# Kernel tuning notes

Measured on AMD Instinct MI355X. Metric: run time of the kernel, lower is better.

## Reference

```python
import jax, jax.numpy as jnp
import numpy as np

EPS = 1e-06


def setup_inputs() -> dict:
    key = jax.random.key(0)
    k1, k2, k3 = jax.random.split(key, 3)
    N, L, H, D = 2, 2048, 8, 64
    return {
        "queries": jax.random.normal(k1, (N, L, H, D), dtype=jnp.float32),
        "keys": jax.random.normal(k2, (N, L, H, D), dtype=jnp.float32),
        "values": jax.random.normal(k3, (N, L, H, D), dtype=jnp.float32),
    }


def reference(queries, keys, values):
    # [N, L, H, D] -> [N, H, L, D]
    q = jnp.transpose(queries, (0, 2, 1, 3))
    k = jnp.transpose(keys, (0, 2, 1, 3))
    v = jnp.transpose(values, (0, 2, 1, 3))
    # kernel_method = sigmoid (applied to q and k only)
    q = jax.nn.sigmoid(q)
    k = jax.nn.sigmoid(k)
    L = q.shape[2]
    normal = (jnp.arange(L, dtype=q.dtype) + 1.0)[None, None, :]  # [1,1,L]

    sink_incoming = 1.0 / jnp.einsum('nhld,nhld->nhl', q + EPS, jnp.cumsum(k, axis=2) + EPS)
    source_outgoing = 1.0 / jnp.einsum('nhld,nhld->nhl', k + EPS, jnp.cumsum(q, axis=2) + EPS)
    sink_incoming = sink_incoming * normal
    source_outgoing = source_outgoing * normal

    conserved_sink = jnp.einsum(
        'nhld,nhld->nhl', q + EPS,
        jnp.cumsum(k * source_outgoing[..., None], axis=2) + EPS) / normal
    conserved_source = jnp.einsum(
        'nhld,nhld->nhl', k + EPS,
        jnp.cumsum(q * sink_incoming[..., None], axis=2) + EPS) / normal
    conserved_source = jnp.clip(conserved_source, -1.0, 1.0)

    sink_allocation = jax.nn.sigmoid(conserved_sink)
    conserved_source = jnp.exp(conserved_source)
    source_competition = conserved_source / jnp.cumsum(conserved_source, axis=-1) * normal

    # causal dot product: outer-product cumsum as in the original
    q_scaled = q * (sink_incoming / normal)[..., None]
    v_scaled = v * source_competition[..., None]
    kv = jnp.cumsum(jnp.einsum('nhld,nhlm->nhldm', k, v_scaled), axis=2)  # [N,H,L,D,M]
    qkv = jnp.einsum('nhld,nhldm->nhlm', q_scaled, kv)
    x = qkv * sink_allocation[..., None]
    # back to [N, L, H, M]
    return jnp.transpose(x, (0, 2, 1, 3))
```

## Files before the change

kernel.cpp:

```cpp
#include <hip/hip_runtime.h>
#include <math.h>

constexpr int Nn = 2, Hh = 8, Ll = 2048, Dd = 64;
constexpr int S  = Nn * Hh;
constexpr int C  = 64;
constexpr int NC = Ll / C;
constexpr int SC = S * NC;

constexpr int SB  = 72;
constexpr int SRP = 65;
constexpr int SS8 = 9;

#define EPSF 1e-6f

typedef __attribute__((ext_vector_type(8))) short short8;
typedef __attribute__((ext_vector_type(4))) float f32x4;
#define MFMA16(a, b, c) __builtin_amdgcn_mfma_f32_16x16x32_bf16(a, b, c, 0, 0, 0)

__device__ __forceinline__ float rcpf(float x) { return __builtin_amdgcn_rcpf(x); }
__device__ __forceinline__ float sigf(float x) { return rcpf(1.0f + __expf(-x)); }

__device__ __forceinline__ float waveRed(float v) {
#pragma unroll
    for (int off = 32; off > 0; off >>= 1) v += __shfl_xor(v, off, 64);
    return v;
}

__device__ __forceinline__ int gidx(int n, int l, int h, int d) {
    return ((n * Ll + l) * Hh + h) * Dd + d;
}

__device__ __forceinline__ float fc(const float4& v, int u) { return ((const float*)&v)[u]; }

__device__ __forceinline__ unsigned short f2bf(float x) {
    unsigned int u = __float_as_uint(x);
    unsigned int r = (u + 0x7fffu + ((u >> 16) & 1u)) >> 16;
    return (unsigned short)r;
}
__device__ __forceinline__ unsigned int pack2(float lo, float hi) {
    return (unsigned int)f2bf(lo) | ((unsigned int)f2bf(hi) << 16);
}
__device__ __forceinline__ float bf2f(unsigned short u) {
    return __uint_as_float(((unsigned int)u) << 16);
}
__device__ __forceinline__ float lo16(unsigned int x) { return __uint_as_float(x << 16); }
__device__ __forceinline__ float hi16(unsigned int x) { return __uint_as_float(x & 0xffff0000u); }
__device__ __forceinline__ void unpack8(const uint4& v, float* o) {
    o[0] = lo16(v.x); o[1] = hi16(v.x); o[2] = lo16(v.y); o[3] = hi16(v.y);
    o[4] = lo16(v.z); o[5] = hi16(v.z); o[6] = lo16(v.w); o[7] = hi16(v.w);
}

__global__ __launch_bounds__(256) void k_stage(const float* __restrict__ Q,
                                               const float* __restrict__ K,
                                               const float* __restrict__ V,
                                               unsigned short* __restrict__ Qb,
                                               unsigned short* __restrict__ Kb,
                                               unsigned short* __restrict__ Kt,
                                               unsigned short* __restrict__ Vt,
                                               float* __restrict__ SK,
                                               float* __restrict__ SQ) {
    __shared__ __align__(16) unsigned short skL[C * SB];
    __shared__ float scr[2048];
    int b = blockIdx.x, s = b / NC, c = b % NC;
    int n = s / Hh, h = s % Hh, t = threadIdx.x;
    int d0 = (4 * t) & 63, ig = t >> 4;
    size_t base = (size_t)b * 4096;
    float psk[4] = {0, 0, 0, 0}, psq[4] = {0, 0, 0, 0};
#pragma unroll
    for (int j = 0; j < 4; j++) {
        int i = ig + 16 * j;
        int id = gidx(n, c * C + i, h, d0);
        float4 q4 = *(const float4*)&Q[id];
        float4 k4 = *(const float4*)&K[id];
        float a0 = sigf(q4.x), a1 = sigf(q4.y), a2 = sigf(q4.z), a3 = sigf(q4.w);
        float b0 = sigf(k4.x), b1 = sigf(k4.y), b2 = sigf(k4.z), b3 = sigf(k4.w);
        uint2 pq2 = make_uint2(pack2(a0, a1), pack2(a2, a3));
        uint2 pk2 = make_uint2(pack2(b0, b1), pack2(b2, b3));
        *(uint2*)&Qb[base + i * 64 + d0] = pq2;
        *(uint2*)&Kb[base + i * 64 + d0] = pk2;
        *(uint2*)&skL[i * SB + d0] = pk2;
        psq[0] += a0; psq[1] += a1; psq[2] += a2; psq[3] += a3;
        psk[0] += b0; psk[1] += b1; psk[2] += b2; psk[3] += b3;
    }
#pragma unroll
    for (int r = 0; r < 4; r++) {
        scr[ig * 64 + d0 + r] = psk[r];
        scr[1024 + ig * 64 + d0 + r] = psq[r];
    }
    __syncthreads();
    if (t < 64) {
        float v = 0.f;
        for (int g = 0; g < 16; g++) v += scr[g * 64 + t];
        SK[b * 64 + t] = v;
    } else if (t < 128) {
        int d = t - 64; float v = 0.f;
        for (int g = 0; g < 16; g++) v += scr[1024 + g * 64 + d];
        SQ[b * 64 + d] = v;
    }
    {
        int i0 = (t & 15) * 4, dt = (t >> 4) * 4;
        uint2 kr[4]; float4 vr[4];
#pragma unroll
        for (int r = 0; r < 4; r++) {
            kr[r] = *(const uint2*)&skL[(i0 + r) * SB + dt];
            vr[r] = *(const float4*)&V[gidx(n, c * C + i0 + r, h, dt)];
        }
#pragma unroll
        for (int u = 0; u < 4; u++) {
            unsigned int e0 = (u < 2 ? kr[0].x : kr[0].y), e1 = (u < 2 ? kr[1].x : kr[1].y);
            unsigned int e2 = (u < 2 ? kr[2].x : kr[2].y), e3 = (u < 2 ? kr[3].x : kr[3].y);
            int sh = (u & 1) * 16;
            unsigned int lo = ((e0 >> sh) & 0xffffu) | (((e1 >> sh) & 0xffffu) << 16);
            unsigned int hi = ((e2 >> sh) & 0xffffu) | (((e3 >> sh) & 0xffffu) << 16);
            *(uint2*)&Kt[base + (dt + u) * 64 + i0] = make_uint2(lo, hi);
            *(uint2*)&Vt[base + (dt + u) * 64 + i0] = make_uint2(
                pack2(fc(vr[0], u), fc(vr[1], u)), pack2(fc(vr[2], u), fc(vr[3], u)));
        }
    }
}

__global__ __launch_bounds__(256) void k_pass1(const unsigned short* __restrict__ Qb,
                                               const unsigned short* __restrict__ Kb,
                                               const float* __restrict__ SK,
                                               const float* __restrict__ SQ,
                                               float* __restrict__ SKso,
                                               float* __restrict__ SQsi,
                                               float* __restrict__ si_g,
                                               float* __restrict__ rw1_g,
                                               float* __restrict__ rw2_g) {
    __shared__ __align__(16) unsigned short sqB[C * SB];
    __shared__ __align__(16) unsigned short skB[C * SB];
    __shared__ float P[C * SRP];
    __shared__ float scrA[C * SS8], scrB[C * SS8];
    __shared__ float colK[C], colQ[C], pk[Dd], pq[Dd], lsi[C], lso[C];
    int b = blockIdx.x, s = b / NC, c = b % NC, t = threadIdx.x;
    size_t base = (size_t)b * 4096;

#pragma unroll
    for (int j = 0; j < 2; j++) {
        int flat = 8 * t + 2048 * j, i = flat >> 6, d0 = flat & 63;
        uint4 xq = *(const uint4*)&Qb[base + flat];
        uint4 xk = *(const uint4*)&Kb[base + flat];
        *(uint4*)&sqB[i * SB + d0] = xq;
        *(uint4*)&skB[i * SB + d0] = xk;
        float qa[8], ka[8];
        unpack8(xq, qa); unpack8(xk, ka);
        float sq = 0.f, sk = 0.f;
#pragma unroll
        for (int u = 0; u < 8; u++) { sq += qa[u]; sk += ka[u]; }
        scrB[i * SS8 + (d0 >> 3)] = sq;
        scrA[i * SS8 + (d0 >> 3)] = sk;
    }
    {
        int d = t & 63, g = t >> 6;
        float pa = 0.f, pb = 0.f;
        for (int cp = g; cp < c; cp += 4) {
            pa += SK[(s * NC + cp) * 64 + d];
            pb += SQ[(s * NC + cp) * 64 + d];
        }
        P[2048 + g * 64 + d] = pa;
        P[2304 + g * 64 + d] = pb;
    }
    __syncthreads();
    if (t < 64) {
        float v = 0.f;
#pragma unroll
        for (int u = 0; u < 8; u++) v += scrA[t * SS8 + u];
        colK[t] = v;
    } else if (t < 128) {
        int i = t - 64; float v = 0.f;
#pragma unroll
        for (int u = 0; u < 8; u++) v += scrB[i * SS8 + u];
        colQ[i] = v;
    } else if (t < 192) {
        int d = t - 128;
        pk[d] = P[2048 + d] + P[2112 + d] + P[2176 + d] + P[2240 + d];
    } else {
        int d = t - 192;
        pq[d] = P[2304 + d] + P[2368 + d] + P[2432 + d] + P[2496 + d];
    }
    __syncthreads();

    {
        int w = t >> 6, lane = t & 63, m = lane & 15, q = lane >> 4;
        f32x4 acc[4] = {{0,0,0,0},{0,0,0,0},{0,0,0,0},{0,0,0,0}};
#pragma unroll
        for (int kk = 0; kk < 64; kk += 32) {
            short8 a = *(const short8*)&sqB[(16 * w + m) * SB + kk + q * 8];
#pragma unroll
            for (int J = 0; J < 4; J++) {
                short8 bb = *(const short8*)&skB[(16 * J + m) * SB + kk + q * 8];
                acc[J] = MFMA16(a, bb, acc[J]);
            }
        }
#pragma unroll
        for (int J = 0; J < 4; J++)
#pragma unroll
            for (int r = 0; r < 4; r++)
                P[(16 * w + 4 * q + r) * SRP + 16 * J + m] = acc[J][r];
    }
    __syncthreads();

    {
        int i = t >> 2, g = t & 3, l = c * C + i;
        float r1 = 0.f, r2 = 0.f;
        for (int jj = g; jj <= i; jj += 4) {
            r1 += P[i * SRP + jj] + EPSF * colK[jj];
            r2 += P[jj * SRP + i] + EPSF * colQ[jj];
        }
        float b1 = 0.f, b2 = 0.f;
#pragma unroll
        for (int u = 0; u < 16; u++) {
            int d = g * 16 + u;
            b1 += (bf2f(sqB[i * SB + d]) + EPSF) * (pk[d] + EPSF);
            b2 += (bf2f(skB[i * SB + d]) + EPSF) * (pq[d] + EPSF);
        }
        r1 += __shfl_xor(r1, 1, 64); r1 += __shfl_xor(r1, 2, 64);
        r2 += __shfl_xor(r2, 1, 64); r2 += __shfl_xor(r2, 2, 64);
        b1 += __shfl_xor(b1, 1, 64); b1 += __shfl_xor(b1, 2, 64);
        b2 += __shfl_xor(b2, 1, 64); b2 += __shfl_xor(b2, 2, 64);
        if (g == 0) {
            float nf = (float)(l + 1);
            float siF = nf * rcpf(b1 + r1), soF = nf * rcpf(b2 + r2);
            si_g[s * Ll + l] = siF;
            lsi[i] = siF; lso[i] = soF;
        }
    }
    __syncthreads();

    {
        int i = t >> 2, g = t & 3;
        float a1 = 0.f, a2 = 0.f;
        for (int jj = g; jj <= i; jj += 4) {
            a1 += lso[jj] * (P[i * SRP + jj] + EPSF * colK[jj]);
            a2 += lsi[jj] * (P[jj * SRP + i] + EPSF * colQ[jj]);
        }
        a1 += __shfl_xor(a1, 1, 64); a1 += __shfl_xor(a1, 2, 64);
        a2 += __shfl_xor(a2, 1, 64); a2 += __shfl_xor(a2, 2, 64);
        if (g == 0) {
            rw1_g[s * Ll + c * C + i] = a1;
            rw2_g[s * Ll + c * C + i] = a2;
        }
    }
    {
        int d = t >> 2, g = t & 3;
        float v1 = 0.f, v2 = 0.f;
#pragma unroll
        for (int u = 0; u < 16; u++) {
            int i = g * 16 + u;
            v1 += bf2f(skB[i * SB + d]) * lso[i];
            v2 += bf2f(sqB[i * SB + d]) * lsi[i];
        }
        v1 += __shfl_xor(v1, 1, 64); v1 += __shfl_xor(v1, 2, 64);
        v2 += __shfl_xor(v2, 1, 64); v2 += __shfl_xor(v2, 2, 64);
        if (g == 0) {
            SKso[b * 64 + d] = v1;
            SQsi[b * 64 + d] = v2;
        }
    }
}

__global__ __launch_bounds__(256) void k_pass2(const unsigned short* __restrict__ Qb,
                                               const unsigned short* __restrict__ Kb,
                                               const float* __restrict__ SKso,
                                               const float* __restrict__ SQsi,
                                               const float* __restrict__ si_g,
                                               const float* __restrict__ rw1_g,
                                               const float* __restrict__ rw2_g,
                                               float* __restrict__ s2_g,
                                               float* __restrict__ e_g,
                                               float* __restrict__ ecum_g,
                                               float* __restrict__ Tcs) {
    __shared__ float scr[512];
    __shared__ float pks[Dd], pqs[Dd], le[C];
    int b = blockIdx.x, s = b / NC, c = b % NC, t = threadIdx.x;

    {
        int d = t & 63, g = t >> 6;
        float pa = 0.f, pb = 0.f;
        for (int cp = g; cp < c; cp += 4) {
            pa += SKso[(s * NC + cp) * 64 + d];
            pb += SQsi[(s * NC + cp) * 64 + d];
        }
        scr[g * 64 + d] = pa;
        scr[256 + g * 64 + d] = pb;
    }
    __syncthreads();
    if (t < 64) pks[t] = scr[t] + scr[64 + t] + scr[128 + t] + scr[192 + t];
    else if (t < 128) {
        int d = t - 64;
        pqs[d] = scr[256 + d] + scr[320 + d] + scr[384 + d] + scr[448 + d];
    }
    __syncthreads();

    int i = t >> 2, g = t & 3, l = c * C + i;
    float b1 = 0.f, b2 = 0.f;
    size_t base = (size_t)b * 4096 + i * 64 + g * 16;
#pragma unroll
    for (int j = 0; j < 2; j++) {
        uint4 xq = *(const uint4*)&Qb[base + 8 * j];
        uint4 xk = *(const uint4*)&Kb[base + 8 * j];
        float qa[8], ka[8];
        unpack8(xq, qa); unpack8(xk, ka);
        int d = g * 16 + 8 * j;
#pragma unroll
        for (int u = 0; u < 8; u++) {
            b1 += (qa[u] + EPSF) * (pks[d + u] + EPSF);
            b2 += (ka[u] + EPSF) * (pqs[d + u] + EPSF);
        }
    }
    b1 += __shfl_xor(b1, 1, 64); b1 += __shfl_xor(b1, 2, 64);
    b2 += __shfl_xor(b2, 1, 64); b2 += __shfl_xor(b2, 2, 64);
    if (g == 0) {
        float nf = (float)(l + 1);
        float cs  = (b1 + rw1_g[s * Ll + l]) * rcpf(nf);
        float csr = (b2 + rw2_g[s * Ll + l]) * rcpf(nf);
        csr = fminf(fmaxf(csr, -1.f), 1.f);
        float e = __expf(csr);
        float sal = sigf(cs);
        s2_g[s * Ll + l] = si_g[s * Ll + l] * rcpf(nf) * sal;
        e_g[s * Ll + l] = e;
        le[i] = e;
    }
    __syncthreads();
    if (t < 64) {
        float run = le[t];
#pragma unroll
        for (int off = 1; off < 64; off <<= 1) {
            float o = __shfl_up(run, off, 64);
            if (t >= off) run += o;
        }
        ecum_g[s * Ll + c * C + t] = run;
        if (t == 63) Tcs[b] = run;
    }
}

__global__ __launch_bounds__(256) void k_kv(const unsigned short* __restrict__ Kt,
                                            const unsigned short* __restrict__ Vt,
                                            const float* __restrict__ e_g,
                                            const float* __restrict__ ecum_g,
                                            const float* __restrict__ Tcs,
                                            float* __restrict__ scomp_g,
                                            float* __restrict__ KVT) {
    __shared__ __align__(16) unsigned short skT[C * SB];
    __shared__ __align__(16) unsigned short vsT[C * SB];
    __shared__ float lsc[C];
    __shared__ float pcsv;
    int b = blockIdx.x, s = b / NC, c = b % NC, t = threadIdx.x;
    if (t < 64) {
        float v = (t < c) ? Tcs[s * NC + t] : 0.f;
        v = waveRed(v);
        if (t == 0) pcsv = v;
    }
    __syncthreads();
    if (t < 64) {
        int l = c * C + t;
        float ls = e_g[s * Ll + l] * rcpf(pcsv + ecum_g[s * Ll + l]) * (float)(l + 1);
        lsc[t] = ls;
        scomp_g[s * Ll + l] = ls;
    }
    __syncthreads();

    size_t base = (size_t)b * 4096;
#pragma unroll
    for (int j = 0; j < 2; j++) {
        int flat = 8 * t + 2048 * j, dR = flat >> 6, i0 = flat & 63;
        *(uint4*)&skT[dR * SB + i0] = *(const uint4*)&Kt[base + flat];
        uint4 vv = *(const uint4*)&Vt[base + flat];
        float x[8];
        unpack8(vv, x);
#pragma unroll
        for (int u = 0; u < 8; u++) x[u] *= lsc[i0 + u];
        uint4 o;
        o.x = pack2(x[0], x[1]); o.y = pack2(x[2], x[3]);
        o.z = pack2(x[4], x[5]); o.w = pack2(x[6], x[7]);
        *(uint4*)&vsT[dR * SB + i0] = o;
    }
    __syncthreads();

    {
        int w = t >> 6, lane = t & 63, m = lane & 15, q = lane >> 4;
        f32x4 acc[4] = {{0,0,0,0},{0,0,0,0},{0,0,0,0},{0,0,0,0}};
#pragma unroll
        for (int kk = 0; kk < 64; kk += 32) {
            short8 a = *(const short8*)&vsT[(16 * w + m) * SB + kk + q * 8];
#pragma unroll
            for (int J = 0; J < 4; J++) {
                short8 bb = *(const short8*)&skT[(16 * J + m) * SB + kk + q * 8];
                acc[J] = MFMA16(a, bb, acc[J]);
            }
        }
#pragma unroll
        for (int J = 0; J < 4; J++)
#pragma unroll
            for (int r = 0; r < 4; r++)
                KVT[(size_t)b * 4096 + (16 * w + 4 * q + r) * 64 + 16 * J + m] = acc[J][r];
    }
}

__global__ __launch_bounds__(256) void k_prefixKV(float* __restrict__ KVT) {
    int bx = blockIdx.x, s = bx >> 4, sub = bx & 15;
    int e0 = sub * 256 + threadIdx.x;
    float x[NC];
#pragma unroll
    for (int cp = 0; cp < NC; cp++)
        x[cp] = KVT[(size_t)(s * NC + cp) * 4096 + e0];
    float r = 0.f;
#pragma unroll
    for (int cp = 0; cp < NC; cp++) {
        float tv = x[cp];
        KVT[(size_t)(s * NC + cp) * 4096 + e0] = r;
        r += tv;
    }
}

__global__ __launch_bounds__(256) void k_final(const unsigned short* __restrict__ Qb,
                                               const unsigned short* __restrict__ Kb,
                                               const unsigned short* __restrict__ Vt,
                                               const float* __restrict__ s2_g,
                                               const float* __restrict__ scomp_g,
                                               const float* __restrict__ KVT,
                                               float* __restrict__ Out) {
    __shared__ __align__(16) unsigned short sqB[C * SB];
    __shared__ __align__(16) unsigned short skB[C * SB];
    __shared__ __align__(16) unsigned short vsT[C * SB];
    __shared__ __align__(16) unsigned short stB[C * SB];
    __shared__ float lsc[C], s2l[C];
    int b = blockIdx.x, s = b / NC, c = b % NC;
    int n = s / Hh, h = s % Hh, t = threadIdx.x;
    int w = t >> 6, lane = t & 63, mf = lane & 15, qq = lane >> 4;
    int I0 = 16 * w;

    if (t < 64) lsc[t] = scomp_g[s * Ll + c * C + t];
    else if (t < 128) s2l[t - 64] = s2_g[s * Ll + c * C + (t - 64)];

    float4 kvr[4];
#pragma unroll
    for (int j = 0; j < 4; j++)
        kvr[j] = *(const float4*)&KVT[(size_t)b * 4096 + 4 * t + 1024 * j];

    size_t base = (size_t)b * 4096;
#pragma unroll
    for (int j = 0; j < 2; j++) {
        int flat = 8 * t + 2048 * j, i = flat >> 6, d0 = flat & 63;
        *(uint4*)&sqB[i * SB + d0] = *(const uint4*)&Qb[base + flat];
        *(uint4*)&skB[i * SB + d0] = *(const uint4*)&Kb[base + flat];
        *(uint4*)&vsT[i * SB + d0] = *(const uint4*)&Vt[base + flat];
    }
    __syncthreads();

    {
        f32x4 acc[4] = {{0,0,0,0},{0,0,0,0},{0,0,0,0},{0,0,0,0}};
#pragma unroll
        for (int kk = 0; kk < 64; kk += 32) {
            short8 a = *(const short8*)&sqB[(I0 + mf) * SB + kk + qq * 8];
#pragma unroll
            for (int J = 0; J < 4; J++) {
                short8 bb = *(const short8*)&skB[(16 * J + mf) * SB + kk + qq * 8];
                acc[J] = MFMA16(a, bb, acc[J]);
            }
        }
#pragma unroll
        for (int J = 0; J < 4; J++)
#pragma unroll
            for (int r = 0; r < 4; r++) {
                int i = I0 + 4 * qq + r, jj = 16 * J + mf;
                float v = (jj <= i) ? acc[J][r] * lsc[jj] : 0.f;
                stB[i * SB + jj] = f2bf(v);
            }
    }
    __syncthreads();

#pragma unroll
    for (int j = 0; j < 4; j++) {
        int flat = 4 * t + 1024 * j, i = flat >> 6, d0 = flat & 63;
        *(uint2*)&skB[i * SB + d0] = make_uint2(pack2(kvr[j].x, kvr[j].y),
                                                pack2(kvr[j].z, kvr[j].w));
    }
    __syncthreads();

    f32x4 acc[4] = {{0,0,0,0},{0,0,0,0},{0,0,0,0},{0,0,0,0}};
#pragma unroll
    for (int kk = 0; kk < 64; kk += 32) {
        short8 a1 = *(const short8*)&sqB[(I0 + mf) * SB + kk + qq * 8];
        short8 a2 = *(const short8*)&stB[(I0 + mf) * SB + kk + qq * 8];
#pragma unroll
        for (int J = 0; J < 4; J++) {
            short8 b1 = *(const short8*)&skB[(16 * J + mf) * SB + kk + qq * 8];
            acc[J] = MFMA16(a1, b1, acc[J]);
            short8 b2 = *(const short8*)&vsT[(16 * J + mf) * SB + kk + qq * 8];
            acc[J] = MFMA16(a2, b2, acc[J]);
        }
    }
#pragma unroll
    for (int J = 0; J < 4; J++)
#pragma unroll
        for (int r = 0; r < 4; r++) {
            int io = I0 + 4 * qq + r;
            Out[gidx(n, c * C + io, h, 16 * J + mf)] = acc[J][r] * s2l[io];
        }
}

extern "C" void kernel_launch(void* const* d_in, const int* in_sizes, int n_in,
                              void* d_out, int out_size, void* d_ws, size_t ws_size,
                              hipStream_t stream) {
    const float* Q = (const float*)d_in[0];
    const float* K = (const float*)d_in[1];
    const float* V = (const float*)d_in[2];
    float* Out = (float*)d_out;

    float* ws    = (float*)d_ws;
    float* SK    = ws;
    float* SQ    = SK    + SC * 64;
    float* SKso  = SQ    + SC * 64;
    float* SQsi  = SKso  + SC * 64;
    float* si_g  = SQsi  + SC * 64;
    float* rw1_g = si_g  + S * Ll;
    float* rw2_g = rw1_g + S * Ll;
    float* s2_g  = rw2_g + S * Ll;
    float* e_g   = s2_g  + S * Ll;
    float* ecum_g= e_g   + S * Ll;
    float* scomp = ecum_g+ S * Ll;
    float* Tcs   = scomp + S * Ll;
    float* KVT   = Tcs   + SC;
    unsigned short* Qb = (unsigned short*)(KVT + (size_t)SC * 4096);
    unsigned short* Kb = Qb + (size_t)SC * 4096;
    unsigned short* Kt = Kb + (size_t)SC * 4096;
    unsigned short* Vt = Kt + (size_t)SC * 4096;

    k_stage<<<SC, 256, 0, stream>>>(Q, K, V, Qb, Kb, Kt, Vt, SK, SQ);
    k_pass1<<<SC, 256, 0, stream>>>(Qb, Kb, SK, SQ, SKso, SQsi, si_g, rw1_g, rw2_g);
    k_pass2<<<SC, 256, 0, stream>>>(Qb, Kb, SKso, SQsi, si_g, rw1_g, rw2_g, s2_g, e_g, ecum_g, Tcs);
    k_kv<<<SC, 256, 0, stream>>>(Kt, Vt, e_g, ecum_g, Tcs, scomp, KVT);
    k_prefixKV<<<256, 256, 0, stream>>>(KVT);
    k_final<<<SC, 256, 0, stream>>>(Qb, Kb, Vt, s2_g, scomp, KVT, Out);
}
```

Measured before the change: 104.0 us.

## Fuse KV prefix scan into final kernel by summing prior chunk states

Removes the separate k_prefixKV launch. Each k_final block now sums the per-chunk KV states of all earlier chunks directly from global memory. Blocks are remapped so the most-loaded chunks (largest c) launch first. This saves one kernel launch and a global read-write pass over KVT, but makes the total reads quadratic in the chunk count (up to 31 chunk states per block) and creates load imbalance between blocks.

```diff
diff --git a/kernel.cpp b/kernel.cpp
--- a/kernel.cpp
+++ b/kernel.cpp
@@ -398,22 +398,6 @@
     }
 }
 
-__global__ __launch_bounds__(256) void k_prefixKV(float* __restrict__ KVT) {
-    int bx = blockIdx.x, s = bx >> 4, sub = bx & 15;
-    int e0 = sub * 256 + threadIdx.x;
-    float x[NC];
-#pragma unroll
-    for (int cp = 0; cp < NC; cp++)
-        x[cp] = KVT[(size_t)(s * NC + cp) * 4096 + e0];
-    float r = 0.f;
-#pragma unroll
-    for (int cp = 0; cp < NC; cp++) {
-        float tv = x[cp];
-        KVT[(size_t)(s * NC + cp) * 4096 + e0] = r;
-        r += tv;
-    }
-}
-
 __global__ __launch_bounds__(256) void k_final(const unsigned short* __restrict__ Qb,
                                                const unsigned short* __restrict__ Kb,
                                                const unsigned short* __restrict__ Vt,
@@ -426,7 +410,9 @@
     __shared__ __align__(16) unsigned short vsT[C * SB];
     __shared__ __align__(16) unsigned short stB[C * SB];
     __shared__ float lsc[C], s2l[C];
-    int b = blockIdx.x, s = b / NC, c = b % NC;
+    int bb = blockIdx.x, s = bb / NC;
+    int c = NC - 1 - (bb % NC);
+    int b = s * NC + c;
     int n = s / Hh, h = s % Hh, t = threadIdx.x;
     int w = t >> 6, lane = t & 63, mf = lane & 15, qq = lane >> 4;
     int I0 = 16 * w;
@@ -434,10 +420,16 @@
     if (t < 64) lsc[t] = scomp_g[s * Ll + c * C + t];
     else if (t < 128) s2l[t - 64] = s2_g[s * Ll + c * C + (t - 64)];
 
-    float4 kvr[4];
-#pragma unroll
-    for (int j = 0; j < 4; j++)
-        kvr[j] = *(const float4*)&KVT[(size_t)b * 4096 + 4 * t + 1024 * j];
+    float4 kvr[4] = {make_float4(0.f, 0.f, 0.f, 0.f), make_float4(0.f, 0.f, 0.f, 0.f),
+                     make_float4(0.f, 0.f, 0.f, 0.f), make_float4(0.f, 0.f, 0.f, 0.f)};
+    for (int cp = 0; cp < c; cp++) {
+        const float* Kp = &KVT[(size_t)(s * NC + cp) * 4096];
+#pragma unroll
+        for (int j = 0; j < 4; j++) {
+            float4 x = *(const float4*)&Kp[4 * t + 1024 * j];
+            kvr[j].x += x.x; kvr[j].y += x.y; kvr[j].z += x.z; kvr[j].w += x.w;
+        }
+    }
 
     size_t base = (size_t)b * 4096;
 #pragma unroll
@@ -456,8 +448,8 @@
             short8 a = *(const short8*)&sqB[(I0 + mf) * SB + kk + qq * 8];
 #pragma unroll
             for (int J = 0; J < 4; J++) {
-                short8 bb = *(const short8*)&skB[(16 * J + mf) * SB + kk + qq * 8];
-                acc[J] = MFMA16(a, bb, acc[J]);
+                short8 bb2 = *(const short8*)&skB[(16 * J + mf) * SB + kk + qq * 8];
+                acc[J] = MFMA16(a, bb2, acc[J]);
             }
         }
 #pragma unroll
@@ -532,6 +524,5 @@
     k_pass1<<<SC, 256, 0, stream>>>(Qb, Kb, SK, SQ, SKso, SQsi, si_g, rw1_g, rw2_g);
     k_pass2<<<SC, 256, 0, stream>>>(Qb, Kb, SKso, SQsi, si_g, rw1_g, rw2_g, s2_g, e_g, ecum_g, Tcs);
     k_kv<<<SC, 256, 0, stream>>>(Kt, Vt, e_g, ecum_g, Tcs, scomp, KVT);
-    k_prefixKV<<<256, 256, 0, stream>>>(KVT);
     k_final<<<SC, 256, 0, stream>>>(Qb, Kb, Vt, s2_g, scomp, KVT, Out);
 }
```

Result: slower. 111.7 us (+7.5%).
